# Optimization experiments

Hardware: AMD Instinct MI355X
Metric: run time of the kernel (lower is better)

The kernel has to match this reference:

```python
import jax, jax.numpy as jnp
import numpy as np

EMB = 1024
HEADS = 16
HEAD_DIM = EMB // HEADS
FF = 4 * EMB
EPS = 1e-5


def setup_inputs() -> dict:
    key = jax.random.key(0)
    ks = jax.random.split(key, 16)
    s = 0.02
    return {
        "x": jax.random.normal(ks[0], (2, 2048, EMB), dtype=jnp.float32),
        "ln1_g": jnp.ones((EMB,), jnp.float32),
        "ln1_b": jnp.zeros((EMB,), jnp.float32),
        "Wq": jax.random.normal(ks[1], (EMB, EMB), jnp.float32) * s,
        "bq": jnp.zeros((EMB,), jnp.float32),
        "Wk": jax.random.normal(ks[2], (EMB, EMB), jnp.float32) * s,
        "bk": jnp.zeros((EMB,), jnp.float32),
        "Wv": jax.random.normal(ks[3], (EMB, EMB), jnp.float32) * s,
        "bv": jnp.zeros((EMB,), jnp.float32),
        "Wo": jax.random.normal(ks[4], (EMB, EMB), jnp.float32) * s,
        "bo": jnp.zeros((EMB,), jnp.float32),
        "ln2_g": jnp.ones((EMB,), jnp.float32),
        "ln2_b": jnp.zeros((EMB,), jnp.float32),
        "W1": jax.random.normal(ks[5], (EMB, FF), jnp.float32) * s,
        "b1": jnp.zeros((FF,), jnp.float32),
        "W2": jax.random.normal(ks[6], (FF, EMB), jnp.float32) * s,
        "b2": jnp.zeros((EMB,), jnp.float32),
    }


def _layernorm(x, g, b):
    mu = jnp.mean(x, axis=-1, keepdims=True)
    var = jnp.var(x, axis=-1, keepdims=True)
    return (x - mu) * jax.lax.rsqrt(var + EPS) * g + b


def _attention(x, Wq, bq, Wk, bk, Wv, bv, Wo, bo):
    B, T, C = x.shape
    # [B,T,C] -> [B,H,T,Dh]
    def split(y):
        return y.reshape(B, T, HEADS, HEAD_DIM).transpose(0, 2, 1, 3)
    Q = split(x @ Wq + bq)
    K = split(x @ Wk + bk)
    V = split(x @ Wv + bv)
    att = jnp.einsum("bhqd,bhkd->bhqk", Q, K) / np.sqrt(HEAD_DIM).astype(np.float32)
    causal = jnp.tril(jnp.ones((T, T), bool))
    att = jnp.where(causal, att, -jnp.inf)
    att = jax.nn.softmax(att, axis=-1)
    out = jnp.einsum("bhqk,bhkd->bhqd", att, V)
    out = out.transpose(0, 2, 1, 3).reshape(B, T, C)
    return out @ Wo + bo


def reference(x, ln1_g, ln1_b, Wq, bq, Wk, bk, Wv, bv, Wo, bo,
              ln2_g, ln2_b, W1, b1, W2, b2):
    # dropout is identity in eval mode
    x = x + _attention(_layernorm(x, ln1_g, ln1_b), Wq, bq, Wk, bk, Wv, bv, Wo, bo)
    h = _layernorm(x, ln2_g, ln2_b)
    h = jax.nn.gelu(h @ W1 + b1, approximate=False) @ W2 + b2
    return x + h
```

## Files before the change

kernel.cpp:

```cpp
#include <hip/hip_runtime.h>
#include <hip/hip_bf16.h>

typedef __attribute__((ext_vector_type(4))) float f32x4;
typedef __attribute__((ext_vector_type(8))) short bf16x8;
typedef unsigned int u32;
typedef unsigned short u16;

#define GASP __attribute__((address_space(1)))
#define LASP __attribute__((address_space(3)))

__device__ __forceinline__ u16 f2bf(float f) {
  u32 u = __float_as_uint(f);
  return (u16)((u + 0x7fffu + ((u >> 16) & 1u)) >> 16);
}

__device__ __forceinline__ u32 cvtpk(float lo, float hi) {
  u32 r;
  asm("v_cvt_pk_bf16_f32 %0, %1, %2" : "=v"(r) : "v"(lo), "v"(hi));
  return r;
}

__device__ __forceinline__ void gl_lds16(const void* g, void* l) {
  __builtin_amdgcn_global_load_lds((const GASP u32*)g, (LASP u32*)l, 16, 0, 0);
}

struct CastArgs {
  const float* s[6];
  u16* d[6];
};

__global__ __launch_bounds__(256) void cast_w(CastArgs a) {
  int bid = blockIdx.x;
  int w, t, K, N, kshift;
  if (bid < 4096)      { w = bid >> 10; t = bid & 1023; K = 1024; N = 1024; kshift = 5; }
  else if (bid < 8192) { w = 4; t = bid - 4096; K = 1024; N = 4096; kshift = 5; }
  else                 { w = 5; t = bid - 8192; K = 4096; N = 1024; kshift = 7; }
  int tk = t & ((1 << kshift) - 1);
  int tn = t >> kshift;
  int k0 = tk << 5, n0 = tn << 5;
  const float* src = a.s[w];
  u16* dst = a.d[w];
  __shared__ u16 tile[32][36];
  int r = threadIdx.x >> 3, c0 = (threadIdx.x & 7) << 2;
  float4 v = *(const float4*)&src[(size_t)(k0 + r) * N + n0 + c0];
  tile[c0 + 0][r] = f2bf(v.x);
  tile[c0 + 1][r] = f2bf(v.y);
  tile[c0 + 2][r] = f2bf(v.z);
  tile[c0 + 3][r] = f2bf(v.w);
  __syncthreads();
  ushort4 o;
  o.x = tile[r][c0 + 0];
  o.y = tile[r][c0 + 1];
  o.z = tile[r][c0 + 2];
  o.w = tile[r][c0 + 3];
  *(ushort4*)&dst[(size_t)(n0 + r) * K + k0 + c0] = o;
}

__global__ __launch_bounds__(256) void ln_k(const float* __restrict__ x, const float* __restrict__ g,
                                            const float* __restrict__ b, u16* __restrict__ out) {
  int row = blockIdx.x;
  int tid = threadIdx.x;
  float4 v = *(const float4*)&x[(size_t)row * 1024 + tid * 4];
  float s = v.x + v.y + v.z + v.w;
  float ss = v.x * v.x + v.y * v.y + v.z * v.z + v.w * v.w;
#pragma unroll
  for (int o = 32; o >= 1; o >>= 1) {
    s += __shfl_xor(s, o, 64);
    ss += __shfl_xor(ss, o, 64);
  }
  __shared__ float red[8];
  int wv = tid >> 6;
  if ((tid & 63) == 0) { red[wv] = s; red[wv + 4] = ss; }
  __syncthreads();
  s = red[0] + red[1] + red[2] + red[3];
  ss = red[4] + red[5] + red[6] + red[7];
  float mu = s * (1.0f / 1024.0f);
  float var = ss * (1.0f / 1024.0f) - mu * mu;
  float rstd = rsqrtf(var + 1e-5f);
  float4 gv = *(const float4*)&g[tid * 4];
  float4 bv = *(const float4*)&b[tid * 4];
  ushort4 o4;
  o4.x = f2bf((v.x - mu) * rstd * gv.x + bv.x);
  o4.y = f2bf((v.y - mu) * rstd * gv.y + bv.y);
  o4.z = f2bf((v.z - mu) * rstd * gv.z + bv.z);
  o4.w = f2bf((v.w - mu) * rstd * gv.w + bv.w);
  *(ushort4*)&out[(size_t)row * 1024 + tid * 4] = o4;
}

template <int MODE>
__global__ __launch_bounds__(512, 2) void gemm_256(
    const u16* __restrict__ A, const u16* __restrict__ Bt,
    const float* __restrict__ bias0, const float* __restrict__ bias1, const float* __restrict__ bias2,
    void* outp, int nbx, int M, int N, int K) {
  __shared__ __align__(16) u16 As[4][128 * 64];
  __shared__ __align__(16) u16 Bs[4][128 * 64];
  char* asB = (char*)As;
  char* bsB = (char*)Bs;
  const int tid = threadIdx.x;
  const int w = tid >> 6, lane = tid & 63;
  const int nwg = gridDim.x;
  const int cpx = nwg >> 3;
  const int sb = (blockIdx.x & 7) * cpx + (blockIdx.x >> 3);
  const int m0 = (sb / nbx) << 8, n0 = (sb % nbx) << 8;

  const int rA = tid >> 3;
  const int csw = ((tid & 7) ^ (rA & 7)) * 8;
  const u16* pA = A + (size_t)(m0 + rA) * K + csw;
  const u16* pB = Bt + (size_t)(n0 + rA) * K + csw;
  const int dstOff = tid * 16;

#define STG_A(kt, h, d_) do {                                            \
    const u16* s_ = pA + (size_t)((h) * 128) * K + (size_t)(kt) * 64;    \
    char* l_ = asB + ((d_) * 2 + (h)) * 16384 + dstOff;                  \
    gl_lds16(s_, l_);                                                    \
    gl_lds16(s_ + (size_t)64 * K, l_ + 8192);                            \
  } while (0)
#define STG_B(kt, h, d_) do {                                            \
    const u16* s_ = pB + (size_t)((h) * 128) * K + (size_t)(kt) * 64;    \
    char* l_ = bsB + ((d_) * 2 + (h)) * 16384 + dstOff;                  \
    gl_lds16(s_, l_);                                                    \
    gl_lds16(s_ + (size_t)64 * K, l_ + 8192);                            \
  } while (0)

  const int wr = w >> 2, wc = w & 3;
  const int g = lane >> 4, qi = lane & 15;

  int aOff[8][2], bOff[4][2];
#pragma unroll
  for (int mm = 0; mm < 8; ++mm) {
    int row = mm * 16 + qi;
#pragma unroll
    for (int ks = 0; ks < 2; ++ks)
      aOff[mm][ks] = row * 128 + (((ks * 4 + g) ^ (qi & 7)) << 4);
  }
#pragma unroll
  for (int nn = 0; nn < 4; ++nn) {
    int rowb = (wc & 1) * 64 + nn * 16 + qi;
#pragma unroll
    for (int ks = 0; ks < 2; ++ks)
      bOff[nn][ks] = rowb * 128 + (((ks * 4 + g) ^ (qi & 7)) << 4);
  }

  f32x4 acc[8][4];
#pragma unroll
  for (int i = 0; i < 8; ++i)
#pragma unroll
    for (int j = 0; j < 4; ++j) acc[i][j] = f32x4{0.f, 0.f, 0.f, 0.f};

#define PHASE(MB) do {                                                                   \
    bf16x8 a00 = *(const bf16x8*)(asB + aTB + aOff[(MB)][0]);                            \
    bf16x8 a01 = *(const bf16x8*)(asB + aTB + aOff[(MB)][1]);                            \
    bf16x8 a10 = *(const bf16x8*)(asB + aTB + aOff[(MB) + 1][0]);                        \
    bf16x8 a11 = *(const bf16x8*)(asB + aTB + aOff[(MB) + 1][1]);                        \
    __builtin_amdgcn_s_setprio(1);                                                       \
    acc[(MB)][0] = __builtin_amdgcn_mfma_f32_16x16x32_bf16(a00, bv[0][0], acc[(MB)][0], 0, 0, 0); \
    acc[(MB)][1] = __builtin_amdgcn_mfma_f32_16x16x32_bf16(a00, bv[1][0], acc[(MB)][1], 0, 0, 0); \
    acc[(MB)][2] = __builtin_amdgcn_mfma_f32_16x16x32_bf16(a00, bv[2][0], acc[(MB)][2], 0, 0, 0); \
    acc[(MB)][3] = __builtin_amdgcn_mfma_f32_16x16x32_bf16(a00, bv[3][0], acc[(MB)][3], 0, 0, 0); \
    acc[(MB) + 1][0] = __builtin_amdgcn_mfma_f32_16x16x32_bf16(a10, bv[0][0], acc[(MB) + 1][0], 0, 0, 0); \
    acc[(MB) + 1][1] = __builtin_amdgcn_mfma_f32_16x16x32_bf16(a10, bv[1][0], acc[(MB) + 1][1], 0, 0, 0); \
    acc[(MB) + 1][2] = __builtin_amdgcn_mfma_f32_16x16x32_bf16(a10, bv[2][0], acc[(MB) + 1][2], 0, 0, 0); \
    acc[(MB) + 1][3] = __builtin_amdgcn_mfma_f32_16x16x32_bf16(a10, bv[3][0], acc[(MB) + 1][3], 0, 0, 0); \
    acc[(MB)][0] = __builtin_amdgcn_mfma_f32_16x16x32_bf16(a01, bv[0][1], acc[(MB)][0], 0, 0, 0); \
    acc[(MB)][1] = __builtin_amdgcn_mfma_f32_16x16x32_bf16(a01, bv[1][1], acc[(MB)][1], 0, 0, 0); \
    acc[(MB)][2] = __builtin_amdgcn_mfma_f32_16x16x32_bf16(a01, bv[2][1], acc[(MB)][2], 0, 0, 0); \
    acc[(MB)][3] = __builtin_amdgcn_mfma_f32_16x16x32_bf16(a01, bv[3][1], acc[(MB)][3], 0, 0, 0); \
    acc[(MB) + 1][0] = __builtin_amdgcn_mfma_f32_16x16x32_bf16(a11, bv[0][1], acc[(MB) + 1][0], 0, 0, 0); \
    acc[(MB) + 1][1] = __builtin_amdgcn_mfma_f32_16x16x32_bf16(a11, bv[1][1], acc[(MB) + 1][1], 0, 0, 0); \
    acc[(MB) + 1][2] = __builtin_amdgcn_mfma_f32_16x16x32_bf16(a11, bv[2][1], acc[(MB) + 1][2], 0, 0, 0); \
    acc[(MB) + 1][3] = __builtin_amdgcn_mfma_f32_16x16x32_bf16(a11, bv[3][1], acc[(MB) + 1][3], 0, 0, 0); \
    __builtin_amdgcn_s_setprio(0);                                                       \
  } while (0)

  const int T = K >> 6;
  STG_A(0, 0, 0); STG_A(0, 1, 0);
  STG_B(0, 0, 0); STG_B(0, 1, 0);
  if (T > 1) { STG_B(1, 0, 1); STG_B(1, 1, 1); }

  for (int t = 0; t < T; ++t) {
    const int d = t & 1;
    const int aTB = (d * 2 + wr) * 16384;
    const int bTB = (d * 2 + (wc >> 1)) * 16384;
    if (t < T - 1) { asm volatile("s_waitcnt vmcnt(4)" ::: "memory"); }
    else           { asm volatile("s_waitcnt vmcnt(0)" ::: "memory"); }
    __builtin_amdgcn_s_barrier();
    asm volatile("" ::: "memory");
    if (t + 1 < T) STG_A(t + 1, 0, d ^ 1);
    bf16x8 bv[4][2];
#pragma unroll
    for (int nn = 0; nn < 4; ++nn) {
      bv[nn][0] = *(const bf16x8*)(bsB + bTB + bOff[nn][0]);
      bv[nn][1] = *(const bf16x8*)(bsB + bTB + bOff[nn][1]);
    }
    PHASE(0);
    __builtin_amdgcn_s_barrier();
    asm volatile("" ::: "memory");
    if (t + 1 < T) STG_A(t + 1, 1, d ^ 1);
    PHASE(2);
    __builtin_amdgcn_s_barrier();
    asm volatile("" ::: "memory");
    if (t + 2 < T) STG_B(t + 2, 0, d);
    PHASE(4);
    __builtin_amdgcn_s_barrier();
    asm volatile("" ::: "memory");
    if (t + 2 < T) STG_B(t + 2, 1, d);
    PHASE(6);
  }
#undef PHASE
#undef STG_A
#undef STG_B

  const int ci = lane & 15;
#pragma unroll
  for (int mm = 0; mm < 8; ++mm) {
#pragma unroll
    for (int nn = 0; nn < 4; ++nn) {
      int colb = n0 + wc * 64 + nn * 16 + ci;
      int rowbase = m0 + wr * 128 + mm * 16 + 4 * g;
      f32x4 c = acc[mm][nn];
      if constexpr (MODE == 2) {
        int sel = colb >> 10;
        int cc = colb & 1023;
        const float* bp = sel == 0 ? bias0 : (sel == 1 ? bias1 : bias2);
        float bb = bp[cc];
        int h = cc >> 6, dd = cc & 63;
        int b_ = rowbase >> 11, tt = rowbase & 2047;
        if (sel == 2) {
          u16* op = (u16*)outp + 2ull * (4096ull * 1024ull);
          ushort4 o4;
          o4.x = f2bf(c[0] + bb);
          o4.y = f2bf(c[1] + bb);
          o4.z = f2bf(c[2] + bb);
          o4.w = f2bf(c[3] + bb);
          *(ushort4*)&op[((size_t)(b_ * 16 + h) * 64 + dd) * 2048 + tt] = o4;
        } else {
          float scale = (sel == 0) ? 0.125f : 1.0f;
          u16* op = (u16*)outp + (size_t)sel * (4096ull * 1024ull);
#pragma unroll
          for (int r = 0; r < 4; ++r)
            op[((size_t)(b_ * 16 + h) * 2048 + tt + r) * 64 + dd] = f2bf((c[r] + bb) * scale);
        }
      } else {
        float bb = bias0[colb];
#pragma unroll
        for (int r = 0; r < 4; ++r) {
          float v = c[r] + bb;
          float gl = 0.5f * v * (1.0f + erff(v * 0.70710678118654752f));
          ((u16*)outp)[(size_t)(rowbase + r) * N + colb] = f2bf(gl);
        }
      }
    }
  }
}

__global__ __launch_bounds__(512) void gemm_sk(
    const u16* __restrict__ A, const u16* __restrict__ Bt,
    const float* __restrict__ bias0, float* __restrict__ outp,
    const float* __restrict__ res, int M, int N, int K) {
  __shared__ __align__(16) union SM {
    struct { u16 As[2][4][128 * 32]; u16 Bs[2][4][128 * 32]; } t;
    float red[16][4][4][64];
  } sm;
  const int tid = threadIdx.x;
  const int w8 = tid >> 6, lane = tid & 63;
  const int gg = w8 >> 2, wl = w8 & 3;
  const int m0 = blockIdx.y << 7, n0 = blockIdx.x << 7;

  char* asB = (char*)sm.t.As[gg];
  char* bsB = (char*)sm.t.Bs[gg];
  const u16* aS[2];
  const u16* bS[2];
#pragma unroll
  for (int i = 0; i < 2; ++i) {
    int p = wl * 2048 + i * 1024 + lane * 16;
    int r = p >> 6;
    int cl = ((p >> 4) & 3) ^ ((r >> 1) & 3);
    aS[i] = A + (size_t)(m0 + r) * K + gg * 32 + cl * 8;
    bS[i] = Bt + (size_t)(n0 + r) * K + gg * 32 + cl * 8;
  }
  f32x4 acc[4][4];
#pragma unroll
  for (int i = 0; i < 4; ++i)
#pragma unroll
    for (int j = 0; j < 4; ++j) acc[i][j] = f32x4{0.f, 0.f, 0.f, 0.f};

  const int wr = wl >> 1, wc = wl & 1;
  int aOff[4], bOff[4];
#pragma unroll
  for (int mm = 0; mm < 4; ++mm) {
    int rowa = wr * 64 + mm * 16 + (lane & 15);
    aOff[mm] = rowa * 64 + (((lane >> 4) ^ ((rowa >> 1) & 3)) << 4);
    int rowb = wc * 64 + mm * 16 + (lane & 15);
    bOff[mm] = rowb * 64 + (((lane >> 4) ^ ((rowb >> 1) & 3)) << 4);
  }

  gl_lds16(aS[0], asB + wl * 2048);
  gl_lds16(aS[1], asB + wl * 2048 + 1024);
  gl_lds16(bS[0], bsB + wl * 2048);
  gl_lds16(bS[1], bsB + wl * 2048 + 1024);
  if (K > 64) {
    gl_lds16(aS[0] + 64, asB + 8192 + wl * 2048);
    gl_lds16(aS[1] + 64, asB + 8192 + wl * 2048 + 1024);
    gl_lds16(bS[0] + 64, bsB + 8192 + wl * 2048);
    gl_lds16(bS[1] + 64, bsB + 8192 + wl * 2048 + 1024);
  }
  if (K > 128) {
    gl_lds16(aS[0] + 128, asB + 16384 + wl * 2048);
    gl_lds16(aS[1] + 128, asB + 16384 + wl * 2048 + 1024);
    gl_lds16(bS[0] + 128, bsB + 16384 + wl * 2048);
    gl_lds16(bS[1] + 128, bsB + 16384 + wl * 2048 + 1024);
  }
  int buf = 0;
  for (int ks = 0; ks < K; ks += 64) {
    const int rem = ((K - ks) >> 6) - 1;
    if (rem >= 2)      { asm volatile("s_waitcnt vmcnt(8)" ::: "memory"); }
    else if (rem == 1) { asm volatile("s_waitcnt vmcnt(4)" ::: "memory"); }
    else               { asm volatile("s_waitcnt vmcnt(0)" ::: "memory"); }
    __builtin_amdgcn_s_barrier();
    asm volatile("" ::: "memory");
    if (ks + 192 < K) {
      const int nb = ((buf + 3) & 3) * 8192;
      gl_lds16(aS[0] + ks + 192, asB + nb + wl * 2048);
      gl_lds16(aS[1] + ks + 192, asB + nb + wl * 2048 + 1024);
      gl_lds16(bS[0] + ks + 192, bsB + nb + wl * 2048);
      gl_lds16(bS[1] + ks + 192, bsB + nb + wl * 2048 + 1024);
    }
    const int tb = buf * 8192;
    bf16x8 av[4], bv[4];
#pragma unroll
    for (int mm = 0; mm < 4; ++mm) av[mm] = *(const bf16x8*)(asB + tb + aOff[mm]);
#pragma unroll
    for (int nn = 0; nn < 4; ++nn) bv[nn] = *(const bf16x8*)(bsB + tb + bOff[nn]);
#pragma unroll
    for (int mm = 0; mm < 4; ++mm)
#pragma unroll
      for (int nn = 0; nn < 4; ++nn)
        acc[mm][nn] = __builtin_amdgcn_mfma_f32_16x16x32_bf16(av[mm], bv[nn], acc[mm][nn], 0, 0, 0);
    buf = (buf + 1) & 3;
  }

  __syncthreads();
  if (gg == 1) {
#pragma unroll
    for (int mm = 0; mm < 4; ++mm)
#pragma unroll
      for (int nn = 0; nn < 4; ++nn)
#pragma unroll
        for (int r = 0; r < 4; ++r) sm.red[mm * 4 + nn][r][wl][lane] = acc[mm][nn][r];
  }
  __syncthreads();
  if (gg == 0) {
    const int g = lane >> 4, ci = lane & 15;
#pragma unroll
    for (int mm = 0; mm < 4; ++mm) {
#pragma unroll
      for (int nn = 0; nn < 4; ++nn) {
        int colb = n0 + wc * 64 + nn * 16 + ci;
        int rowbase = m0 + wr * 64 + mm * 16 + 4 * g;
        float bb = bias0[colb];
#pragma unroll
        for (int r = 0; r < 4; ++r) {
          size_t idx = (size_t)(rowbase + r) * N + colb;
          outp[idx] = acc[mm][nn][r] + sm.red[mm * 4 + nn][r][wl][lane] + bb + res[idx];
        }
      }
    }
  }
}

__global__ __launch_bounds__(512) void attn_k(const u16* __restrict__ Q, const u16* __restrict__ Kg,
                                              const u16* __restrict__ Vt, u16* __restrict__ O) {
  __shared__ __align__(16) u16 Ks[2][64 * 64];
  __shared__ __align__(16) u16 Vs[2][64 * 64];
  const int bx = blockIdx.y;
  const int bh = blockIdx.x;
  const int tid = threadIdx.x, w = tid >> 6, lane = tid & 63;
  const int g = lane >> 4, qi = lane & 15;
  const u16* Qb = Q + (size_t)bh * 2048 * 64;
  const u16* Kb = Kg + (size_t)bh * 2048 * 64;
  const u16* Vtb = Vt + (size_t)bh * 64 * 2048;

  const int rS = tid >> 3, cS = tid & 7;
  const int csw = (cS ^ (rS & 7)) * 8;
  const u16* srcK = Kb + (size_t)rS * 64 + csw;
  const u16* srcV = Vtb + (size_t)rS * 2048 + csw;
  char* ksB = (char*)Ks;
  char* vsB = (char*)Vs;
  const int dstOff = tid * 16;

  int koff[4][2], voff[4][2];
#pragma unroll
  for (int t = 0; t < 4; ++t) {
    int row = 16 * t + qi;
#pragma unroll
    for (int h = 0; h < 2; ++h) koff[t][h] = row * 128 + (((4 * h + g) ^ (qi & 7)) << 4);
#pragma unroll
    for (int kt = 0; kt < 2; ++kt) voff[t][kt] = row * 128 + (((4 * kt + g) ^ (qi & 7)) << 4);
  }

  const int b_ = bh >> 4, hh = bh & 15;
  u32* Ou = (u32*)O;

  for (int job = 0; job < 2; ++job) {
    const int qt = job ? bx : 15 - bx;
    const int qmin = qt * 128 + w * 16;
    const int qrow = qmin + qi;
    const int qmaxw = qmin + 15;

    bf16x8 qf[2];
#pragma unroll
    for (int h = 0; h < 2; ++h)
      qf[h] = *(const bf16x8*)(Qb + (size_t)qrow * 64 + h * 32 + g * 8);

    f32x4 acc[4];
#pragma unroll
    for (int dt = 0; dt < 4; ++dt) acc[dt] = f32x4{0.f, 0.f, 0.f, 0.f};
    float m = -1e30f, lsum = 0.0f;

    __syncthreads();
    gl_lds16(srcK, ksB + dstOff);
    gl_lds16(srcV, vsB + dstOff);

    const int nsteps = 2 * qt + 2;
    int buf = 0;
    for (int s = 0; s < nsteps; ++s) {
      __syncthreads();
      if (s + 1 < nsteps) {
        int nb = buf ^ 1;
        gl_lds16(srcK + (size_t)(s + 1) * 4096, ksB + nb * 8192 + dstOff);
        gl_lds16(srcV + (size_t)(s + 1) * 64, vsB + nb * 8192 + dstOff);
      }
      const int kv0 = s * 64;
      if (kv0 <= qmaxw) {
        const int tb = buf * 8192;
        f32x4 st[4];
        __builtin_amdgcn_s_setprio(1);
#pragma unroll
        for (int t = 0; t < 4; ++t) {
          st[t] = f32x4{0.f, 0.f, 0.f, 0.f};
#pragma unroll
          for (int h = 0; h < 2; ++h) {
            bf16x8 kf = *(const bf16x8*)(ksB + tb + koff[t][h]);
            st[t] = __builtin_amdgcn_mfma_f32_16x16x32_bf16(kf, qf[h], st[t], 0, 0, 0);
          }
        }
        __builtin_amdgcn_s_setprio(0);
        float pvv[4][4];
        float tmax = -1e30f;
        if (kv0 + 63 > qmin) {
#pragma unroll
          for (int t = 0; t < 4; ++t)
#pragma unroll
            for (int r = 0; r < 4; ++r) {
              int key = kv0 + 16 * t + 4 * g + r;
              float sv = st[t][r];
              sv = (key <= qrow) ? sv : -1e30f;
              pvv[t][r] = sv;
              tmax = fmaxf(tmax, sv);
            }
        } else {
#pragma unroll
          for (int t = 0; t < 4; ++t)
#pragma unroll
            for (int r = 0; r < 4; ++r) {
              float sv = st[t][r];
              pvv[t][r] = sv;
              tmax = fmaxf(tmax, sv);
            }
        }
        tmax = fmaxf(tmax, __shfl_xor(tmax, 16, 64));
        tmax = fmaxf(tmax, __shfl_xor(tmax, 32, 64));
        if (!__all(tmax <= m + 8.0f)) {
          float mn = fmaxf(m, tmax);
          float corr = __expf(m - mn);
          lsum *= corr;
#pragma unroll
          for (int dt = 0; dt < 4; ++dt)
#pragma unroll
            for (int r = 0; r < 4; ++r) acc[dt][r] *= corr;
          m = mn;
        }
        float tsum = 0.f;
#pragma unroll
        for (int t = 0; t < 4; ++t)
#pragma unroll
          for (int r = 0; r < 4; ++r) {
            float e = __expf(pvv[t][r] - m);
            pvv[t][r] = e;
            tsum += e;
          }
        tsum += __shfl_xor(tsum, 16, 64);
        tsum += __shfl_xor(tsum, 32, 64);
        lsum += tsum;
        u32 pk[4][2], ex[4][2];
#pragma unroll
        for (int t = 0; t < 4; ++t)
#pragma unroll
          for (int p = 0; p < 2; ++p) {
            u32 v = cvtpk(pvv[t][2 * p], pvv[t][2 * p + 1]);
            pk[t][p] = v;
            ex[t][p] = (u32)__shfl_xor((int)v, 16, 64);
          }
        const bool ge = (g & 1) == 0;
        const bool G0 = (g >> 1) == 0;
        const bool innr = (g == 0) || (g == 3);
        u32 mm_[4][4];
#pragma unroll
        for (int t = 0; t < 4; ++t) {
          mm_[t][0] = ge ? pk[t][0] : ex[t][0];
          mm_[t][1] = ge ? pk[t][1] : ex[t][1];
          mm_[t][2] = ge ? ex[t][0] : pk[t][0];
          mm_[t][3] = ge ? ex[t][1] : pk[t][1];
        }
        union Frag { u32 u[4]; bf16x8 v; } f0, f1;
#pragma unroll
        for (int i = 0; i < 4; ++i) {
          u32 sel0 = G0 ? mm_[1][i] : mm_[0][i];
          u32 sel1 = G0 ? mm_[3][i] : mm_[2][i];
          u32 sw0 = (u32)__shfl_xor((int)sel0, 32, 64);
          u32 sw1 = (u32)__shfl_xor((int)sel1, 32, 64);
          u32 own0 = G0 ? mm_[0][i] : mm_[1][i];
          u32 own1 = G0 ? mm_[2][i] : mm_[3][i];
          f0.u[i] = innr ? own0 : sw0;
          f1.u[i] = innr ? own1 : sw1;
        }
        __builtin_amdgcn_s_setprio(1);
#pragma unroll
        for (int dt = 0; dt < 4; ++dt) {
          bf16x8 vfa = *(const bf16x8*)(vsB + tb + voff[dt][0]);
          acc[dt] = __builtin_amdgcn_mfma_f32_16x16x32_bf16(vfa, f0.v, acc[dt], 0, 0, 0);
          bf16x8 vfb = *(const bf16x8*)(vsB + tb + voff[dt][1]);
          acc[dt] = __builtin_amdgcn_mfma_f32_16x16x32_bf16(vfb, f1.v, acc[dt], 0, 0, 0);
        }
        __builtin_amdgcn_s_setprio(0);
      }
      buf ^= 1;
    }

    float rl = 1.0f / lsum;
    size_t rowq = (size_t)(b_ * 2048 + qrow);
#pragma unroll
    for (int dt = 0; dt < 4; ++dt) {
#pragma unroll
      for (int rp = 0; rp < 2; ++rp) {
        u16 lo = f2bf(acc[dt][rp * 2] * rl);
        u16 hi = f2bf(acc[dt][rp * 2 + 1] * rl);
        u32 pkd = (u32)lo | ((u32)hi << 16);
        size_t off = rowq * 1024 + hh * 64 + dt * 16 + 4 * g + rp * 2;
        Ou[off >> 1] = pkd;
      }
    }
  }
}

extern "C" void kernel_launch(void* const* d_in, const int* in_sizes, int n_in,
                              void* d_out, int out_size, void* d_ws, size_t ws_size,
                              hipStream_t stream) {
  const float* x    = (const float*)d_in[0];
  const float* ln1g = (const float*)d_in[1];
  const float* ln1b = (const float*)d_in[2];
  const float* Wq   = (const float*)d_in[3];
  const float* bq   = (const float*)d_in[4];
  const float* Wk   = (const float*)d_in[5];
  const float* bk   = (const float*)d_in[6];
  const float* Wv   = (const float*)d_in[7];
  const float* bv   = (const float*)d_in[8];
  const float* Wo   = (const float*)d_in[9];
  const float* bo   = (const float*)d_in[10];
  const float* ln2g = (const float*)d_in[11];
  const float* ln2b = (const float*)d_in[12];
  const float* W1   = (const float*)d_in[13];
  const float* b1   = (const float*)d_in[14];
  const float* W2   = (const float*)d_in[15];
  const float* b2   = (const float*)d_in[16];

  char* ws = (char*)d_ws;
  const size_t MB = 1ull << 20;
  u16* WqT = (u16*)(ws + 0 * MB);
  u16* WkT = (u16*)(ws + 2 * MB);
  u16* WvT = (u16*)(ws + 4 * MB);
  u16* WoT = (u16*)(ws + 6 * MB);
  u16* W1T = (u16*)(ws + 8 * MB);
  u16* W2T = (u16*)(ws + 16 * MB);
  u16* XN  = (u16*)(ws + 24 * MB);
  u16* Qb  = (u16*)(ws + 32 * MB);
  u16* Kb  = (u16*)(ws + 40 * MB);
  u16* Vtb = (u16*)(ws + 48 * MB);
  u16* Ob  = (u16*)(ws + 56 * MB);
  u16* Gb  = (u16*)(ws + 32 * MB);

  CastArgs ca;
  ca.s[0] = Wq; ca.s[1] = Wk; ca.s[2] = Wv; ca.s[3] = Wo; ca.s[4] = W1; ca.s[5] = W2;
  ca.d[0] = WqT; ca.d[1] = WkT; ca.d[2] = WvT; ca.d[3] = WoT; ca.d[4] = W1T; ca.d[5] = W2T;
  cast_w<<<12288, 256, 0, stream>>>(ca);

  ln_k<<<4096, 256, 0, stream>>>(x, ln1g, ln1b, XN);

  gemm_256<2><<<12 * 16, 512, 0, stream>>>(XN, WqT, bq, bk, bv, Qb, 12, 4096, 3072, 1024);

  attn_k<<<dim3(32, 8), 512, 0, stream>>>(Qb, Kb, Vtb, Ob);

  gemm_sk<<<dim3(8, 32), 512, 0, stream>>>(Ob, WoT, bo, (float*)d_out, x, 4096, 1024, 1024);

  ln_k<<<4096, 256, 0, stream>>>((const float*)d_out, ln2g, ln2b, XN);

  gemm_256<3><<<16 * 16, 512, 0, stream>>>(XN, W1T, b1, nullptr, nullptr, Gb, 16, 4096, 4096, 1024);

  gemm_sk<<<dim3(8, 32), 512, 0, stream>>>(Gb, W2T, b2, (float*)d_out, (const float*)d_out, 4096, 1024, 4096);
}
```

Baseline: 247.5 us.

## Reschedule GEMM LDS reads before barriers and tile-group blocks per XCD

Each phase of the 256x256 GEMM now issues its LDS A-fragment reads before the barrier and the next async global-to-LDS stage, then runs its MFMAs. The vmcnt wait moves to the end of the iteration, with a prologue wait added. The aim is to overlap LDS latency with the barrier and stage issue. Block-to-tile mapping changes from a linear swizzle to a 2D rectangular grouping per XCD (rm x rn tiles), so each XCD's L2 reuses its A and B panels. This adds register pressure from fragments held across barriers and depends on the grid and rm/rn/xn parameters being consistent.

```diff
diff --git a/kernel.cpp b/kernel.cpp
--- a/kernel.cpp
+++ b/kernel.cpp
@@ -91,17 +91,17 @@
 __global__ __launch_bounds__(512, 2) void gemm_256(
     const u16* __restrict__ A, const u16* __restrict__ Bt,
     const float* __restrict__ bias0, const float* __restrict__ bias1, const float* __restrict__ bias2,
-    void* outp, int nbx, int M, int N, int K) {
+    void* outp, int rm, int rn, int xn, int M, int N, int K) {
   __shared__ __align__(16) u16 As[4][128 * 64];
   __shared__ __align__(16) u16 Bs[4][128 * 64];
   char* asB = (char*)As;
   char* bsB = (char*)Bs;
   const int tid = threadIdx.x;
   const int w = tid >> 6, lane = tid & 63;
-  const int nwg = gridDim.x;
-  const int cpx = nwg >> 3;
-  const int sb = (blockIdx.x & 7) * cpx + (blockIdx.x >> 3);
-  const int m0 = (sb / nbx) << 8, n0 = (sb % nbx) << 8;
+  const int xcd = blockIdx.x & 7, idx = blockIdx.x >> 3;
+  const int mt = (xcd / xn) * rm + (idx % rm);
+  const int nt = (xcd % xn) * rn + (idx / rm);
+  const int m0 = mt << 8, n0 = nt << 8;
 
   const int rA = tid >> 3;
   const int csw = ((tid & 7) ^ (rA & 7)) * 8;
@@ -147,66 +147,89 @@
 #pragma unroll
     for (int j = 0; j < 4; ++j) acc[i][j] = f32x4{0.f, 0.f, 0.f, 0.f};
 
-#define PHASE(MB) do {                                                                   \
-    bf16x8 a00 = *(const bf16x8*)(asB + aTB + aOff[(MB)][0]);                            \
-    bf16x8 a01 = *(const bf16x8*)(asB + aTB + aOff[(MB)][1]);                            \
-    bf16x8 a10 = *(const bf16x8*)(asB + aTB + aOff[(MB) + 1][0]);                        \
-    bf16x8 a11 = *(const bf16x8*)(asB + aTB + aOff[(MB) + 1][1]);                        \
+#define MFMA16(MB, A00, A01, A10, A11) do {                                              \
     __builtin_amdgcn_s_setprio(1);                                                       \
-    acc[(MB)][0] = __builtin_amdgcn_mfma_f32_16x16x32_bf16(a00, bv[0][0], acc[(MB)][0], 0, 0, 0); \
-    acc[(MB)][1] = __builtin_amdgcn_mfma_f32_16x16x32_bf16(a00, bv[1][0], acc[(MB)][1], 0, 0, 0); \
-    acc[(MB)][2] = __builtin_amdgcn_mfma_f32_16x16x32_bf16(a00, bv[2][0], acc[(MB)][2], 0, 0, 0); \
-    acc[(MB)][3] = __builtin_amdgcn_mfma_f32_16x16x32_bf16(a00, bv[3][0], acc[(MB)][3], 0, 0, 0); \
-    acc[(MB) + 1][0] = __builtin_amdgcn_mfma_f32_16x16x32_bf16(a10, bv[0][0], acc[(MB) + 1][0], 0, 0, 0); \
-    acc[(MB) + 1][1] = __builtin_amdgcn_mfma_f32_16x16x32_bf16(a10, bv[1][0], acc[(MB) + 1][1], 0, 0, 0); \
-    acc[(MB) + 1][2] = __builtin_amdgcn_mfma_f32_16x16x32_bf16(a10, bv[2][0], acc[(MB) + 1][2], 0, 0, 0); \
-    acc[(MB) + 1][3] = __builtin_amdgcn_mfma_f32_16x16x32_bf16(a10, bv[3][0], acc[(MB) + 1][3], 0, 0, 0); \
-    acc[(MB)][0] = __builtin_amdgcn_mfma_f32_16x16x32_bf16(a01, bv[0][1], acc[(MB)][0], 0, 0, 0); \
-    acc[(MB)][1] = __builtin_amdgcn_mfma_f32_16x16x32_bf16(a01, bv[1][1], acc[(MB)][1], 0, 0, 0); \
-    acc[(MB)][2] = __builtin_amdgcn_mfma_f32_16x16x32_bf16(a01, bv[2][1], acc[(MB)][2], 0, 0, 0); \
-    acc[(MB)][3] = __builtin_amdgcn_mfma_f32_16x16x32_bf16(a01, bv[3][1], acc[(MB)][3], 0, 0, 0); \
-    acc[(MB) + 1][0] = __builtin_amdgcn_mfma_f32_16x16x32_bf16(a11, bv[0][1], acc[(MB) + 1][0], 0, 0, 0); \
-    acc[(MB) + 1][1] = __builtin_amdgcn_mfma_f32_16x16x32_bf16(a11, bv[1][1], acc[(MB) + 1][1], 0, 0, 0); \
-    acc[(MB) + 1][2] = __builtin_amdgcn_mfma_f32_16x16x32_bf16(a11, bv[2][1], acc[(MB) + 1][2], 0, 0, 0); \
-    acc[(MB) + 1][3] = __builtin_amdgcn_mfma_f32_16x16x32_bf16(a11, bv[3][1], acc[(MB) + 1][3], 0, 0, 0); \
+    acc[(MB)][0] = __builtin_amdgcn_mfma_f32_16x16x32_bf16(A00, bv[0][0], acc[(MB)][0], 0, 0, 0); \
+    acc[(MB)][1] = __builtin_amdgcn_mfma_f32_16x16x32_bf16(A00, bv[1][0], acc[(MB)][1], 0, 0, 0); \
+    acc[(MB)][2] = __builtin_amdgcn_mfma_f32_16x16x32_bf16(A00, bv[2][0], acc[(MB)][2], 0, 0, 0); \
+    acc[(MB)][3] = __builtin_amdgcn_mfma_f32_16x16x32_bf16(A00, bv[3][0], acc[(MB)][3], 0, 0, 0); \
+    acc[(MB) + 1][0] = __builtin_amdgcn_mfma_f32_16x16x32_bf16(A10, bv[0][0], acc[(MB) + 1][0], 0, 0, 0); \
+    acc[(MB) + 1][1] = __builtin_amdgcn_mfma_f32_16x16x32_bf16(A10, bv[1][0], acc[(MB) + 1][1], 0, 0, 0); \
+    acc[(MB) + 1][2] = __builtin_amdgcn_mfma_f32_16x16x32_bf16(A10, bv[2][0], acc[(MB) + 1][2], 0, 0, 0); \
+    acc[(MB) + 1][3] = __builtin_amdgcn_mfma_f32_16x16x32_bf16(A10, bv[3][0], acc[(MB) + 1][3], 0, 0, 0); \
+    acc[(MB)][0] = __builtin_amdgcn_mfma_f32_16x16x32_bf16(A01, bv[0][1], acc[(MB)][0], 0, 0, 0); \
+    acc[(MB)][1] = __builtin_amdgcn_mfma_f32_16x16x32_bf16(A01, bv[1][1], acc[(MB)][1], 0, 0, 0); \
+    acc[(MB)][2] = __builtin_amdgcn_mfma_f32_16x16x32_bf16(A01, bv[2][1], acc[(MB)][2], 0, 0, 0); \
+    acc[(MB)][3] = __builtin_amdgcn_mfma_f32_16x16x32_bf16(A01, bv[3][1], acc[(MB)][3], 0, 0, 0); \
+    acc[(MB) + 1][0] = __builtin_amdgcn_mfma_f32_16x16x32_bf16(A11, bv[0][1], acc[(MB) + 1][0], 0, 0, 0); \
+    acc[(MB) + 1][1] = __builtin_amdgcn_mfma_f32_16x16x32_bf16(A11, bv[1][1], acc[(MB) + 1][1], 0, 0, 0); \
+    acc[(MB) + 1][2] = __builtin_amdgcn_mfma_f32_16x16x32_bf16(A11, bv[2][1], acc[(MB) + 1][2], 0, 0, 0); \
+    acc[(MB) + 1][3] = __builtin_amdgcn_mfma_f32_16x16x32_bf16(A11, bv[3][1], acc[(MB) + 1][3], 0, 0, 0); \
     __builtin_amdgcn_s_setprio(0);                                                       \
   } while (0)
+
+#define RDA(dst0, dst1, MB)                                          \
+    bf16x8 dst0##0 = *(const bf16x8*)(asB + aTB + aOff[(MB)][0]);     \
+    bf16x8 dst0##1 = *(const bf16x8*)(asB + aTB + aOff[(MB)][1]);     \
+    bf16x8 dst1##0 = *(const bf16x8*)(asB + aTB + aOff[(MB) + 1][0]); \
+    bf16x8 dst1##1 = *(const bf16x8*)(asB + aTB + aOff[(MB) + 1][1]);
 
   const int T = K >> 6;
   STG_A(0, 0, 0); STG_A(0, 1, 0);
   STG_B(0, 0, 0); STG_B(0, 1, 0);
-  if (T > 1) { STG_B(1, 0, 1); STG_B(1, 1, 1); }
+  if (T > 1) {
+    STG_B(1, 0, 1); STG_B(1, 1, 1);
+    asm volatile("s_waitcnt vmcnt(4)" ::: "memory");
+  } else {
+    asm volatile("s_waitcnt vmcnt(0)" ::: "memory");
+  }
+  __builtin_amdgcn_s_barrier();
 
   for (int t = 0; t < T; ++t) {
     const int d = t & 1;
     const int aTB = (d * 2 + wr) * 16384;
     const int bTB = (d * 2 + (wc >> 1)) * 16384;
-    if (t < T - 1) { asm volatile("s_waitcnt vmcnt(4)" ::: "memory"); }
-    else           { asm volatile("s_waitcnt vmcnt(0)" ::: "memory"); }
-    __builtin_amdgcn_s_barrier();
-    asm volatile("" ::: "memory");
-    if (t + 1 < T) STG_A(t + 1, 0, d ^ 1);
     bf16x8 bv[4][2];
 #pragma unroll
     for (int nn = 0; nn < 4; ++nn) {
       bv[nn][0] = *(const bf16x8*)(bsB + bTB + bOff[nn][0]);
       bv[nn][1] = *(const bf16x8*)(bsB + bTB + bOff[nn][1]);
     }
-    PHASE(0);
+    RDA(p0a, p0b, 0);
+    asm volatile("" ::: "memory");
+    if (t + 1 < T) STG_A(t + 1, 0, d ^ 1);
     __builtin_amdgcn_s_barrier();
-    asm volatile("" ::: "memory");
-    if (t + 1 < T) STG_A(t + 1, 1, d ^ 1);
-    PHASE(2);
+    MFMA16(0, p0a0, p0a1, p0b0, p0b1);
     __builtin_amdgcn_s_barrier();
-    asm volatile("" ::: "memory");
-    if (t + 2 < T) STG_B(t + 2, 0, d);
-    PHASE(4);
-    __builtin_amdgcn_s_barrier();
-    asm volatile("" ::: "memory");
-    if (t + 2 < T) STG_B(t + 2, 1, d);
-    PHASE(6);
-  }
-#undef PHASE
+    {
+      RDA(p1a, p1b, 2);
+      asm volatile("" ::: "memory");
+      if (t + 1 < T) STG_A(t + 1, 1, d ^ 1);
+      __builtin_amdgcn_s_barrier();
+      MFMA16(2, p1a0, p1a1, p1b0, p1b1);
+      __builtin_amdgcn_s_barrier();
+    }
+    {
+      RDA(p2a, p2b, 4);
+      asm volatile("" ::: "memory");
+      if (t + 2 < T) STG_B(t + 2, 0, d);
+      __builtin_amdgcn_s_barrier();
+      MFMA16(4, p2a0, p2a1, p2b0, p2b1);
+      __builtin_amdgcn_s_barrier();
+    }
+    {
+      RDA(p3a, p3b, 6);
+      asm volatile("" ::: "memory");
+      if (t + 2 < T) STG_B(t + 2, 1, d);
+      __builtin_amdgcn_s_barrier();
+      MFMA16(6, p3a0, p3a1, p3b0, p3b1);
+      if (t < T - 2)       { asm volatile("s_waitcnt vmcnt(4)" ::: "memory"); }
+      else if (t == T - 2) { asm volatile("s_waitcnt vmcnt(0)" ::: "memory"); }
+      __builtin_amdgcn_s_barrier();
+    }
+  }
+#undef MFMA16
+#undef RDA
 #undef STG_A
 #undef STG_B
 
@@ -596,7 +619,7 @@
 
   ln_k<<<4096, 256, 0, stream>>>(x, ln1g, ln1b, XN);
 
-  gemm_256<2><<<12 * 16, 512, 0, stream>>>(XN, WqT, bq, bk, bv, Qb, 12, 4096, 3072, 1024);
+  gemm_256<2><<<192, 512, 0, stream>>>(XN, WqT, bq, bk, bv, Qb, 4, 6, 2, 4096, 3072, 1024);
 
   attn_k<<<dim3(32, 8), 512, 0, stream>>>(Qb, Kb, Vtb, Ob);
 
@@ -604,7 +627,7 @@
 
   ln_k<<<4096, 256, 0, stream>>>((const float*)d_out, ln2g, ln2b, XN);
 
-  gemm_256<3><<<16 * 16, 512, 0, stream>>>(XN, W1T, b1, nullptr, nullptr, Gb, 16, 4096, 4096, 1024);
+  gemm_256<3><<<256, 512, 0, stream>>>(XN, W1T, b1, nullptr, nullptr, Gb, 8, 4, 4, 4096, 4096, 1024);
 
   gemm_sk<<<dim3(8, 32), 512, 0, stream>>>(Gb, W2T, b2, (float*)d_out, (const float*)d_out, 4096, 1024, 4096);
 }
```

Measured after the change: 239.2 us. 1.03x faster.
